# Kernel tuning notes

Measured on AMD Instinct MI355X. Metric: run time of the kernel, lower is better.

Reference implementation:

```python
import jax, jax.numpy as jnp
import numpy as np

N_NODES = 1024
HID = 128
NODE_D = 133
BOND_D = 14
E_HALF = 8192  # directed edges; doubled with reverses -> 16384


def setup_inputs() -> dict:
    key = jax.random.key(0)
    ks = jax.random.split(key, 24)

    x = jax.random.normal(ks[0], (N_NODES, NODE_D), jnp.float32)
    edge_attr = jax.random.normal(ks[1], (2 * E_HALF, BOND_D), jnp.float32)
    src = jax.random.randint(ks[2], (E_HALF,), 0, N_NODES)
    dst = jax.random.randint(ks[3], (E_HALF,), 0, N_NODES)
    # bidirectional edges so every edge has a reverse (as _rev_edge_index assumes)
    edge_index = jnp.stack([jnp.concatenate([src, dst]), jnp.concatenate([dst, src])]).astype(jnp.int32)
    rev_edge_index = jnp.concatenate([jnp.arange(E_HALF) + E_HALF, jnp.arange(E_HALF)]).astype(jnp.int32)

    dissociable_masks = (jax.random.uniform(ks[4], (N_NODES,)) < 0.1).astype(jnp.int32)
    pka_raw = jax.random.uniform(ks[5], (N_NODES,), minval=0.0, maxval=14.0)
    valid = jax.random.uniform(ks[6], (N_NODES,)) < (1.0 / 16.0)
    pka_values = jnp.where(valid, pka_raw, jnp.nan).astype(jnp.float32)

    def lin(k, fi, fo):
        return (jax.random.normal(k, (fi, fo)) / np.sqrt(fi)).astype(jnp.float32)

    z = lambda n: jnp.zeros((n,), jnp.float32)
    inp = dict(x=x, edge_attr=edge_attr, pka_values=pka_values,
               dissociable_masks=dissociable_masks, edge_index=edge_index,
               rev_edge_index=rev_edge_index,
               Wi=lin(ks[7], NODE_D + BOND_D, HID), bi=z(HID),
               Wh=lin(ks[8], HID, HID), bh=z(HID),
               Wo=lin(ks[9], NODE_D + HID, HID), bo=z(HID),
               Wnt=lin(ks[10], NODE_D, HID), bnt=z(HID),
               Wc1=lin(ks[11], HID, 256), bc1=z(256),
               Wc2=lin(ks[12], 256, 64), bc2=z(64),
               Wc3=lin(ks[13], 64, 2), bc3=z(2),
               Wr1=lin(ks[14], HID, 256), br1=z(256),
               Wr2=lin(ks[15], 256, 64), br2=z(64),
               Wr3=lin(ks[16], 64, 1), br3=z(1),
               Wg=lin(ks[17], HID, HID), bg=z(HID))
    return inp


def reference(x, edge_attr, pka_values, dissociable_masks, edge_index, rev_edge_index,
              Wi, bi, Wh, bh, Wo, bo, Wnt, bnt,
              Wc1, bc1, Wc2, bc2, Wc3, bc3,
              Wr1, br1, Wr2, br2, Wr3, br3, Wg, bg):
    n = x.shape[0]
    src, dst = edge_index[0], edge_index[1]

    # ---- BondMessagePassing (depth=3, dropout in eval mode) ----
    H0 = jnp.concatenate([x[src], edge_attr], axis=1) @ Wi + bi  # [E, HID]
    Ht = jax.nn.relu(H0)
    for _ in range(2):  # depth - 1 iterations
        agg = jax.ops.segment_sum(Ht, dst, num_segments=n)       # scatter-sum to dst
        M = agg[src] - Ht[rev_edge_index]                        # exclude reverse edge
        Ht = jax.nn.relu(H0 + M @ Wh + bh)
    agg = jax.ops.segment_sum(Ht, dst, num_segments=n)
    tx = x @ Wnt + bnt
    M = jnp.where(jnp.sum(agg, axis=1, keepdims=True) == 0, tx, agg)
    E = jax.nn.relu(jnp.concatenate([x, M], axis=1) @ Wo + bo)   # node embeddings [N, HID]

    valid = ~jnp.isnan(pka_values)
    pka_s = jnp.where(valid, pka_values, 0.0)

    def mlp(e, W1, b1, W2, b2, W3, b3):
        h = jax.nn.relu(e @ W1 + b1)
        h = jax.nn.relu(h @ W2 + b2)
        return h @ W3 + b3

    def step(carry, inp):
        Emb, cls_sum, reg_sum, correct = carry
        i, m_i, p_i, v_i = inp
        e = Emb[i]
        logits = mlp(e, Wc1, bc1, Wc2, bc2, Wc3, bc3)            # [2]
        label = jnp.argmax(logits).astype(jnp.int32)
        target = (m_i > 0).astype(jnp.int32)
        ce = -jax.nn.log_softmax(logits)[target]
        correct = correct + (label == target).astype(jnp.float32)
        reg_cond = (label == 1) | (m_i > 0)
        # sigmoid -> Hardtanh(0,14) (clip is identity on (0,1), kept for fidelity)
        p = jnp.clip(jax.nn.sigmoid(mlp(e, Wr1, br1, Wr2, br2, Wr3, br3))[0], 0.0, 14.0)
        fire = reg_cond & v_i
        reg_sum = reg_sum + jnp.where(fire, (p - p_i) ** 2, 0.0)
        Emb = jax.lax.cond(fire,
                           lambda A: A * (1.0 - jax.nn.sigmoid(A @ Wg + bg)),
                           lambda A: A, Emb)
        return (Emb, cls_sum + ce, reg_sum, correct), (label, jnp.where(reg_cond, p, 0.0))

    init = (E, jnp.float32(0.0), jnp.float32(0.0), jnp.float32(0.0))
    xs = (jnp.arange(n), dissociable_masks, pka_s, valid)
    (_, cls_sum, reg_sum, correct), (labels, preds) = jax.lax.scan(step, init, xs)
    acc = jax.lax.stop_gradient(correct / n)
    loss_vec = jnp.stack([cls_sum + reg_sum, cls_sum, reg_sum, acc])
    return labels, preds, loss_vec
```

## Files before the change

kernel.cpp:

```cpp
#include <hip/hip_runtime.h>

#define NN   1024
#define NE   16384
#define HID  128
#define ND   133
#define BD   14
#define KIN  147
#define NVMAX 128
#define EB   8
#define JF   4
#define JT   2
#define MAXPAIRS (NVMAX * (NVMAX + 1) / 2)
#define TB4 ((MAXPAIRS + JT - 1) / JT)

__device__ __forceinline__ float sigm(float x) { return 1.0f / (1.0f + expf(-x)); }


__global__ void __launch_bounds__(1024)
k_prep3(const int* __restrict__ dst, int* offs, int* elist,
        const float* __restrict__ pka, int* validIdx, int* NvP, int* vpos,
        const int* __restrict__ mask, int* pairCnt, int* pairList,
        int* lossTicket) {
    __shared__ int degS[NN];
    __shared__ int s2[NN];
    __shared__ int fillS[NN];
    __shared__ int elistS[NE];
    __shared__ int vIdxS[NVMAX];
    __shared__ int maskS[NVMAX];
    __shared__ int nvS, pcS;
    int t = threadIdx.x;
    degS[t] = 0;
    float v = pka[t];
    int f = (v == v) ? 1 : 0;
    s2[t] = f;
    __syncthreads();
    for (int e = t; e < NE; e += NN) atomicAdd(&degS[dst[e]], 1);
    __syncthreads();
    int d0 = degS[t];
    __syncthreads();
    for (int st = 1; st < NN; st <<= 1) {
        int a = (t >= st) ? degS[t - st] : 0;
        int b = (t >= st) ? s2[t - st] : 0;
        __syncthreads();
        degS[t] += a; s2[t] += b;
        __syncthreads();
    }
    int hi = degS[t];
    int lo = hi - d0;
    offs[t] = lo;
    fillS[t] = lo;
    if (t == NN - 1) offs[NN] = hi;
    int pos = s2[t] - f;
    int ok = (f && pos < NVMAX) ? 1 : 0;
    vpos[t] = ok ? pos : -1;
    if (ok) { validIdx[pos] = t; vIdxS[pos] = t; }
    if (t == NN - 1) { int nv = (s2[t] > NVMAX) ? NVMAX : s2[t]; *NvP = nv; nvS = nv; }
    if (t == 0) { pcS = 0; *lossTicket = 0; }
    __syncthreads();
    for (int e = t; e < NE; e += NN) { int p = atomicAdd(&fillS[dst[e]], 1); elistS[p] = e; }
    int Nv = nvS;
    if (t < NVMAX) maskS[t] = (t < Nv) ? mask[vIdxS[t]] : 1;
    __syncthreads();
    for (int a = lo + 1; a < hi; a++) {
        int vv = elistS[a]; int b = a - 1;
        while (b >= lo && elistS[b] > vv) { elistS[b + 1] = elistS[b]; b--; }
        elistS[b + 1] = vv;
    }
    for (int idx = t; idx < NVMAX * NVMAX; idx += NN) {
        int vv = idx >> 7, k = idx & (NVMAX - 1);
        if (vv < Nv && k <= vv && maskS[vv] == 0) {
            int p = atomicAdd(&pcS, 1);
            pairList[p] = idx;
        }
    }
    __syncthreads();
    if (t == 0) *pairCnt = pcS;
    for (int e = t; e < NE; e += NN) elist[e] = elistS[e];
}


__global__ void k_edge_init(const float* __restrict__ x, const float* __restrict__ ea,
                            const int* __restrict__ src,
                            const float* __restrict__ Wi, const float* __restrict__ bi,
                            float* __restrict__ H0, float* __restrict__ Ht) {
    __shared__ float in[EB][KIN + 1];
    int e0 = blockIdx.x * EB;
    int h = threadIdx.x;
    for (int j = 0; j < EB; j++) {
        int e = e0 + j; int s = src[e];
        for (int k = h; k < KIN; k += HID)
            in[j][k] = (k < ND) ? x[s * ND + k] : ea[e * BD + (k - ND)];
    }
    __syncthreads();
    float acc[EB];
#pragma unroll
    for (int j = 0; j < EB; j++) acc[j] = 0.f;
    for (int k = 0; k < KIN; k++) {
        float w = Wi[k * HID + h];
#pragma unroll
        for (int j = 0; j < EB; j++) acc[j] = fmaf(in[j][k], w, acc[j]);
    }
    float b = bi[h];
    for (int j = 0; j < EB; j++) {
        float v = acc[j] + b;
        H0[(e0 + j) * HID + h] = v;
        Ht[(e0 + j) * HID + h] = fmaxf(v, 0.f);
    }
}

__global__ void k_segsum(const float* __restrict__ Ht, const int* __restrict__ elist,
                         const int* __restrict__ offs, float* __restrict__ agg) {
    int n = blockIdx.x; int h = threadIdx.x;
    int lo = offs[n], hi = offs[n + 1];
    float a = 0.f;
    for (int j = lo; j < hi; j++) {
        int e = elist[j];
        a += Ht[e * HID + h];
    }
    agg[n * HID + h] = a;
}

__global__ void k_edge_update(const float* __restrict__ H0, const float* __restrict__ Htin,
                              const float* __restrict__ agg,
                              const int* __restrict__ src, const int* __restrict__ rev,
                              const float* __restrict__ Wh, const float* __restrict__ bh,
                              float* __restrict__ Htout) {
    __shared__ float M[EB][HID];
    int e0 = blockIdx.x * EB;
    int h = threadIdx.x;
    for (int j = 0; j < EB; j++) {
        int e = e0 + j; int s = src[e]; int r = rev[e];
        M[j][h] = agg[s * HID + h] - Htin[r * HID + h];
    }
    __syncthreads();
    float acc[EB];
#pragma unroll
    for (int j = 0; j < EB; j++) acc[j] = 0.f;
    for (int k = 0; k < HID; k++) {
        float w = Wh[k * HID + h];
#pragma unroll
        for (int j = 0; j < EB; j++) acc[j] = fmaf(M[j][k], w, acc[j]);
    }
    float b = bh[h];
    for (int j = 0; j < EB; j++) {
        int e = e0 + j;
        Htout[e * HID + h] = fmaxf(H0[e * HID + h] + acc[j] + b, 0.f);
    }
}

__global__ void k_node_embed2(const float* __restrict__ x, const float* __restrict__ Ht,
                              const int* __restrict__ elist, const int* __restrict__ offs,
                              const float* __restrict__ Wnt, const float* __restrict__ bnt,
                              const float* __restrict__ Wo, const float* __restrict__ bo,
                              float* __restrict__ Emb) {
    __shared__ float xs[ND + 1];
    __shared__ float Ms[HID];
    __shared__ float red[HID];
    int n = blockIdx.x; int h = threadIdx.x;
    for (int k = h; k < ND; k += HID) xs[k] = x[n * ND + k];
    int lo = offs[n], hi = offs[n + 1];
    float a = 0.f;
    for (int j = lo; j < hi; j++) a += Ht[elist[j] * HID + h];
    red[h] = a;
    __syncthreads();
    for (int st = 64; st > 0; st >>= 1) { if (h < st) red[h] += red[h + st]; __syncthreads(); }
    float s = red[0];
    __syncthreads();
    float Mh;
    if (s == 0.0f) {
        float t0 = 0.f, t1 = 0.f;
        int k = 0;
        for (; k + 1 < ND; k += 2) {
            t0 = fmaf(xs[k], Wnt[k * HID + h], t0);
            t1 = fmaf(xs[k + 1], Wnt[(k + 1) * HID + h], t1);
        }
        for (; k < ND; k++) t0 = fmaf(xs[k], Wnt[k * HID + h], t0);
        Mh = (t0 + t1) + bnt[h];
    } else {
        Mh = a;
    }
    Ms[h] = Mh;
    __syncthreads();
    float a0 = 0.f, a1 = 0.f;
    int k = 0;
    for (; k + 1 < ND; k += 2) {
        a0 = fmaf(xs[k], Wo[k * HID + h], a0);
        a1 = fmaf(xs[k + 1], Wo[(k + 1) * HID + h], a1);
    }
    for (; k < ND; k++) a0 = fmaf(xs[k], Wo[k * HID + h], a0);
    for (int q = 0; q < HID; q += 2) {
        a0 = fmaf(Ms[q], Wo[(ND + q) * HID + h], a0);
        a1 = fmaf(Ms[q + 1], Wo[(ND + q + 1) * HID + h], a1);
    }
    Emb[n * HID + h] = fmaxf((a0 + a1) + bo[h], 0.f);
}


__global__ void __launch_bounds__(512)
k_chains3(const float* __restrict__ Emb, const int* __restrict__ validIdx,
          const int* __restrict__ NvP,
          const float* __restrict__ Wg, const float* __restrict__ bg,
          float* __restrict__ specSt) {
    int v = blockIdx.x;
    int Nv = *NvP;
    if (v >= Nv) return;
    __shared__ float rS[HID];
    __shared__ float pS[512];
    int tid = threadIdx.x;
    int col = tid & (HID - 1);
    int slot = tid >> 7;
    float wreg[32];
#pragma unroll
    for (int q = 0; q < 32; q++)
        wreg[q] = Wg[(slot * 32 + q) * HID + col];
    float bgc = bg[col];
    int i = validIdx[v];
    if (tid < HID) rS[tid] = Emb[i * HID + tid];
    __syncthreads();
    if (slot == 0) specSt[(size_t)(v * NVMAX + 0) * HID + col] = rS[col];
    int kmax = (v < NVMAX - 1) ? v : (NVMAX - 1);
    for (int k = 1; k <= kmax; k++) {
        const float4* r4 = (const float4*)&rS[slot * 32];
        float px = 0.f, py = 0.f, pz = 0.f, pw = 0.f;
#pragma unroll
        for (int q8 = 0; q8 < 8; q8++) {
            float4 rr = r4[q8];
            px = fmaf(rr.x, wreg[4 * q8 + 0], px);
            py = fmaf(rr.y, wreg[4 * q8 + 1], py);
            pz = fmaf(rr.z, wreg[4 * q8 + 2], pz);
            pw = fmaf(rr.w, wreg[4 * q8 + 3], pw);
        }
        pS[tid] = (px + py) + (pz + pw);
        __syncthreads();
        if (slot == 0) {
            float s = ((pS[col] + pS[col + 128]) + (pS[col + 256] + pS[col + 384])) + bgc;
            float g = 1.0f - sigm(s);
            float nr = rS[col] * g;
            rS[col] = nr;
            specSt[(size_t)(v * NVMAX + k) * HID + col] = nr;
        }
        __syncthreads();
    }
}


__global__ void __launch_bounds__(256)
k_table4(const float* __restrict__ specSt, const int* __restrict__ pairList,
         const int* __restrict__ pairCnt,
         const float* __restrict__ Wc1, const float* __restrict__ bc1,
         const float* __restrict__ Wc2, const float* __restrict__ bc2,
         const float* __restrict__ Wc3, const float* __restrict__ bc3,
         int* __restrict__ labTab) {
    int cnt = *pairCnt;
    int base = blockIdx.x * JT;
    if (base >= cnt) return;
    int nj = cnt - base; if (nj > JT) nj = JT;
    __shared__ float rS[JT][HID];
    __shared__ float h1S[JT][256];
    __shared__ float h2S[JT][64];
    __shared__ int plS[JT];
    int tid = threadIdx.x;
    if (tid < JT) plS[tid] = (tid < nj) ? pairList[base + tid] : 0;
    __syncthreads();
    for (int idx = tid; idx < JT * HID; idx += 256) {
        int j = idx >> 7, k = idx & (HID - 1);
        rS[j][k] = (j < nj) ? specSt[(size_t)plS[j] * HID + k] : 0.f;
    }
    __syncthreads();
    {
        float a[JT];
#pragma unroll
        for (int j = 0; j < JT; j++) a[j] = 0.f;
        for (int k = 0; k < HID; k++) {
            float w = Wc1[k * 256 + tid];
#pragma unroll
            for (int j = 0; j < JT; j++) a[j] = fmaf(rS[j][k], w, a[j]);
        }
        float b1 = bc1[tid];
#pragma unroll
        for (int j = 0; j < JT; j++) h1S[j][tid] = fmaxf(a[j] + b1, 0.f);
    }
    __syncthreads();
    {
        int col = tid & 63, j = tid >> 6;
        if (j < nj) {
            float acc = 0.f;
            for (int k = 0; k < 256; k++)
                acc = fmaf(h1S[j][k], Wc2[k * 64 + col], acc);
            h2S[j][col] = fmaxf(acc + bc2[col], 0.f);
        }
    }
    __syncthreads();
    if (tid < nj) {
        float l0 = bc3[0], l1 = bc3[1];
        for (int k = 0; k < 64; k++) {
            float h = h2S[tid][k];
            l0 = fmaf(h, Wc3[2 * k + 0], l0);
            l1 = fmaf(h, Wc3[2 * k + 1], l1);
        }
        labTab[plS[tid]] = (l1 > l0) ? 1 : 0;
    }
}


__global__ void k_resolve2(const int* __restrict__ validIdx, const int* __restrict__ NvP,
                           const int* __restrict__ mask, const int* __restrict__ labTab,
                           int* fireFlag, int* kPref) {
    __shared__ int vIdxS[NVMAX];
    __shared__ int maskS[NVMAX];
    __shared__ int labS[NVMAX * NVMAX];
    __shared__ int fireS[NN];
    __shared__ int scanS[NN];
    int t = threadIdx.x;
    int Nv = *NvP;
    if (t < NVMAX) {
        int vi = (t < Nv) ? validIdx[t] : 0;
        vIdxS[t] = vi;
        maskS[t] = (t < Nv) ? mask[vi] : 0;
    }
    fireS[t] = 0;
    for (int idx = t; idx < Nv * NVMAX; idx += NN) labS[idx] = labTab[idx];
    __syncthreads();
    if (t == 0) {
        int k = 0;
        for (int v = 0; v < Nv; v++) {
            int fire = (maskS[v] > 0) ? 1 : labS[v * NVMAX + k];
            fireS[vIdxS[v]] = fire;
            k += fire;
        }
    }
    __syncthreads();
    int f0 = fireS[t];
    scanS[t] = f0;
    __syncthreads();
    for (int st = 1; st < NN; st <<= 1) {
        int u = (t >= st) ? scanS[t - st] : 0;
        __syncthreads();
        scanS[t] += u;
        __syncthreads();
    }
    kPref[t] = scanS[t] - f0;
    fireFlag[t] = f0;
}


__global__ void __launch_bounds__(256)
k_final4(const float* __restrict__ Emb, const int* __restrict__ kPref,
         const int* __restrict__ fireFlag, const int* __restrict__ mask,
         const float* __restrict__ pka, const int* __restrict__ vpos,
         const int* __restrict__ labTab,
         const float* __restrict__ Wg, const float* __restrict__ bg,
         const float* __restrict__ Wc1, const float* __restrict__ bc1,
         const float* __restrict__ Wc2, const float* __restrict__ bc2,
         const float* __restrict__ Wc3, const float* __restrict__ bc3,
         const float* __restrict__ Wr1, const float* __restrict__ br1,
         const float* __restrict__ Wr2, const float* __restrict__ br2,
         const float* __restrict__ Wr3, const float* __restrict__ br3,
         float* __restrict__ outLabels, float* __restrict__ outPreds,
         float* __restrict__ ceArr, float* __restrict__ regArr,
         float* __restrict__ corArr, float* __restrict__ outLoss,
         int* __restrict__ lossTicket) {
    __shared__ float WgS[HID * HID];
    __shared__ float rS[JF][HID];
    __shared__ float h1S[JF][256];
    __shared__ float h2S[JF][64];
    __shared__ float lgS[JF][2];
    __shared__ float prS[JF];
    __shared__ int kcS[JF];
    __shared__ int tkS;
    int tid = threadIdx.x;
    int i0 = blockIdx.x * JF;

    const float4* Wg4 = (const float4*)Wg;
    float4* Ws4 = (float4*)WgS;
    for (int idx = tid; idx < HID * HID / 4; idx += 256) Ws4[idx] = Wg4[idx];
    if (tid < HID) {
#pragma unroll
        for (int j = 0; j < JF; j++) rS[j][tid] = Emb[(i0 + j) * HID + tid];
    }
    if (tid < JF) kcS[tid] = kPref[i0 + tid];
    __syncthreads();
    int kc[JF]; int maxkc = 0;
#pragma unroll
    for (int j = 0; j < JF; j++) { kc[j] = kcS[j]; if (kc[j] > maxkc) maxkc = kc[j]; }

    int col = tid & (HID - 1);
    int slot = tid >> 7;
    int j0 = slot * 2, j1 = slot * 2 + 1;
    float bgc = bg[col];
    for (int t = 0; t < maxkc; t++) {
        float a00 = 0.f, a01 = 0.f, a02 = 0.f, a03 = 0.f;
        float a10 = 0.f, a11 = 0.f, a12 = 0.f, a13 = 0.f;
        for (int q = 0; q < HID; q += 4) {
            float w0 = WgS[(q + 0) * HID + col];
            float w1 = WgS[(q + 1) * HID + col];
            float w2 = WgS[(q + 2) * HID + col];
            float w3 = WgS[(q + 3) * HID + col];
            a00 = fmaf(rS[j0][q + 0], w0, a00);
            a01 = fmaf(rS[j0][q + 1], w1, a01);
            a02 = fmaf(rS[j0][q + 2], w2, a02);
            a03 = fmaf(rS[j0][q + 3], w3, a03);
            a10 = fmaf(rS[j1][q + 0], w0, a10);
            a11 = fmaf(rS[j1][q + 1], w1, a11);
            a12 = fmaf(rS[j1][q + 2], w2, a12);
            a13 = fmaf(rS[j1][q + 3], w3, a13);
        }
        float g0 = 1.0f - sigm(((a00 + a01) + (a02 + a03)) + bgc);
        float g1 = 1.0f - sigm(((a10 + a11) + (a12 + a13)) + bgc);
        __syncthreads();
        if (t < kc[j0]) rS[j0][col] *= g0;
        if (t < kc[j1]) rS[j1][col] *= g1;
        __syncthreads();
    }

    {
        float a[JF];
#pragma unroll
        for (int j = 0; j < JF; j++) a[j] = 0.f;
        for (int k = 0; k < HID; k++) {
            float w = Wc1[k * 256 + tid];
#pragma unroll
            for (int j = 0; j < JF; j++) a[j] = fmaf(rS[j][k], w, a[j]);
        }
        float b = bc1[tid];
#pragma unroll
        for (int j = 0; j < JF; j++) h1S[j][tid] = fmaxf(a[j] + b, 0.f);
    }
    __syncthreads();
    {
        int c2 = tid & 63, j = tid >> 6;
        float acc = 0.f;
        for (int k = 0; k < 256; k++) acc = fmaf(h1S[j][k], Wc2[k * 64 + c2], acc);
        h2S[j][c2] = fmaxf(acc + bc2[c2], 0.f);
    }
    __syncthreads();
    if (tid < 2 * JF) {
        int j = tid >> 1, c = tid & 1;
        float l = bc3[c];
        for (int k = 0; k < 64; k++) l = fmaf(h2S[j][k], Wc3[2 * k + c], l);
        lgS[j][c] = l;
    }
    __syncthreads();

    {
        float a[JF];
#pragma unroll
        for (int j = 0; j < JF; j++) a[j] = 0.f;
        for (int k = 0; k < HID; k++) {
            float w = Wr1[k * 256 + tid];
#pragma unroll
            for (int j = 0; j < JF; j++) a[j] = fmaf(rS[j][k], w, a[j]);
        }
        float b = br1[tid];
#pragma unroll
        for (int j = 0; j < JF; j++) h1S[j][tid] = fmaxf(a[j] + b, 0.f);
    }
    __syncthreads();
    {
        int c2 = tid & 63, j = tid >> 6;
        float acc = 0.f;
        for (int k = 0; k < 256; k++) acc = fmaf(h1S[j][k], Wr2[k * 64 + c2], acc);
        h2S[j][c2] = fmaxf(acc + br2[c2], 0.f);
    }
    __syncthreads();
    if (tid < JF) {
        float pr = br3[0];
        for (int k = 0; k < 64; k++) pr = fmaf(h2S[tid][k], Wr3[k], pr);
        prS[tid] = pr;
    }
    __syncthreads();

    if (tid < JF) {
        int j = tid, i = i0 + j;
        float l0 = lgS[j][0], l1 = lgS[j][1];
        int compLab = (l1 > l0) ? 1 : 0;
        int vp = vpos[i];
        int label = (vp >= 0 && mask[i] == 0) ? labTab[vp * NVMAX + kc[j]] : compLab;
        int target = (mask[i] > 0) ? 1 : 0;
        float mx = fmaxf(l0, l1);
        float lse = mx + logf(expf(l0 - mx) + expf(l1 - mx));
        float ce = lse - ((target == 1) ? l1 : l0);
        int reg_cond = (label == 1) || (mask[i] > 0);
        float p = sigm(prS[j]);
        p = fminf(fmaxf(p, 0.f), 14.f);
        outLabels[i] = (float)label;
        outPreds[i] = reg_cond ? p : 0.f;
        ceArr[i] = ce;
        corArr[i] = (label == target) ? 1.f : 0.f;
        if (fireFlag[i]) {
            float d = p - pka[i];
            regArr[i] = d * d;
        } else {
            regArr[i] = 0.f;
        }
    }

    __threadfence();
    __syncthreads();
    if (tid == 0) tkS = atomicAdd(lossTicket, 1);
    __syncthreads();
    if (tkS == (NN / JF) - 1) {
        __threadfence();
        __shared__ float s[256];
        float a = ((ceArr[tid] + ceArr[tid + 256]) + (ceArr[tid + 512] + ceArr[tid + 768]));
        s[tid] = a; __syncthreads();
        for (int st = 128; st > 0; st >>= 1) { if (tid < st) s[tid] += s[tid + st]; __syncthreads(); }
        float cls = s[0]; __syncthreads();
        a = ((regArr[tid] + regArr[tid + 256]) + (regArr[tid + 512] + regArr[tid + 768]));
        s[tid] = a; __syncthreads();
        for (int st = 128; st > 0; st >>= 1) { if (tid < st) s[tid] += s[tid + st]; __syncthreads(); }
        float reg = s[0]; __syncthreads();
        a = ((corArr[tid] + corArr[tid + 256]) + (corArr[tid + 512] + corArr[tid + 768]));
        s[tid] = a; __syncthreads();
        for (int st = 128; st > 0; st >>= 1) { if (tid < st) s[tid] += s[tid + st]; __syncthreads(); }
        float cor = s[0];
        if (tid == 0) {
            outLoss[0] = cls + reg;
            outLoss[1] = cls;
            outLoss[2] = reg;
            outLoss[3] = cor / (float)NN;
        }
    }
}


extern "C" void kernel_launch(void* const* d_in, const int* in_sizes, int n_in,
                              void* d_out, int out_size, void* d_ws, size_t ws_size,
                              hipStream_t stream) {
    const float* x    = (const float*)d_in[0];
    const float* ea   = (const float*)d_in[1];
    const float* pka  = (const float*)d_in[2];
    const int*   mask = (const int*)d_in[3];
    const int*   eidx = (const int*)d_in[4];
    const int*   rev  = (const int*)d_in[5];
    const float* Wi  = (const float*)d_in[6];  const float* bi  = (const float*)d_in[7];
    const float* Wh  = (const float*)d_in[8];  const float* bh  = (const float*)d_in[9];
    const float* Wo  = (const float*)d_in[10]; const float* bo  = (const float*)d_in[11];
    const float* Wnt = (const float*)d_in[12]; const float* bnt = (const float*)d_in[13];
    const float* Wc1 = (const float*)d_in[14]; const float* bc1 = (const float*)d_in[15];
    const float* Wc2 = (const float*)d_in[16]; const float* bc2 = (const float*)d_in[17];
    const float* Wc3 = (const float*)d_in[18]; const float* bc3 = (const float*)d_in[19];
    const float* Wr1 = (const float*)d_in[20]; const float* br1 = (const float*)d_in[21];
    const float* Wr2 = (const float*)d_in[22]; const float* br2 = (const float*)d_in[23];
    const float* Wr3 = (const float*)d_in[24]; const float* br3 = (const float*)d_in[25];
    const float* Wg  = (const float*)d_in[26]; const float* bg  = (const float*)d_in[27];

    const int* src = eidx;
    const int* dst = eidx + NE;

    char* w = (char*)d_ws;
    auto alloc = [&](size_t bytes) -> void* {
        void* p = (void*)w;
        w += ((bytes + 255) / 256) * 256;
        return p;
    };
    float* H0   = (float*)alloc((size_t)NE * HID * 4);
    float* HtA  = (float*)alloc((size_t)NE * HID * 4);
    float* HtB  = (float*)alloc((size_t)NE * HID * 4);
    float* agg  = (float*)alloc((size_t)NN * HID * 4);
    float* Emb  = (float*)alloc((size_t)NN * HID * 4);
    int* offs    = (int*)alloc((NN + 1) * 4);
    int* elist   = (int*)alloc(NE * 4);
    int* validIdx= (int*)alloc(NVMAX * 4);
    int* NvP     = (int*)alloc(16);
    int* vpos    = (int*)alloc(NN * 4);
    int* fireFlag= (int*)alloc(NN * 4);
    int* kPref   = (int*)alloc(NN * 4);
    float* specSt= (float*)alloc((size_t)NVMAX * NVMAX * HID * 4);
    int* labTab  = (int*)alloc(NVMAX * NVMAX * 4);
    int* pairCnt = (int*)alloc(16);
    int* pairList= (int*)alloc(MAXPAIRS * 4);
    int* lossTicket = (int*)alloc(16);
    float* ceArr = (float*)alloc(NN * 4);
    float* regArr= (float*)alloc(NN * 4);
    float* corArr= (float*)alloc(NN * 4);

    float* outF = (float*)d_out;

    k_prep3<<<1, NN, 0, stream>>>(dst, offs, elist, pka, validIdx, NvP, vpos,
                                  mask, pairCnt, pairList, lossTicket);

    k_edge_init<<<NE / EB, HID, 0, stream>>>(x, ea, src, Wi, bi, H0, HtA);
    k_segsum<<<NN, HID, 0, stream>>>(HtA, elist, offs, agg);
    k_edge_update<<<NE / EB, HID, 0, stream>>>(H0, HtA, agg, src, rev, Wh, bh, HtB);
    k_segsum<<<NN, HID, 0, stream>>>(HtB, elist, offs, agg);
    k_edge_update<<<NE / EB, HID, 0, stream>>>(H0, HtB, agg, src, rev, Wh, bh, HtA);
    k_node_embed2<<<NN, HID, 0, stream>>>(x, HtA, elist, offs, Wnt, bnt, Wo, bo, Emb);

    k_chains3<<<NVMAX, 512, 0, stream>>>(Emb, validIdx, NvP, Wg, bg, specSt);
    k_table4<<<TB4, 256, 0, stream>>>(specSt, pairList, pairCnt,
                                      Wc1, bc1, Wc2, bc2, Wc3, bc3, labTab);
    k_resolve2<<<1, NN, 0, stream>>>(validIdx, NvP, mask, labTab, fireFlag, kPref);

    k_final4<<<NN / JF, 256, 0, stream>>>(Emb, kPref, fireFlag, mask, pka, vpos, labTab,
                                          Wg, bg, Wc1, bc1, Wc2, bc2, Wc3, bc3,
                                          Wr1, br1, Wr2, br2, Wr3, br3,
                                          outF, outF + NN, ceArr, regArr, corArr,
                                          outF + 2 * NN, lossTicket);
}
```

Baseline: 223.3 us.

## Hold Wg gate weights in registers and split final kernel into smaller blocks

```diff
diff --git a/kernel.cpp b/kernel.cpp
--- a/kernel.cpp
+++ b/kernel.cpp
@@ -8,10 +8,11 @@
 #define KIN  147
 #define NVMAX 128
 #define EB   8
-#define JF   4
+#define JF   2
 #define JT   2
 #define MAXPAIRS (NVMAX * (NVMAX + 1) / 2)
 #define TB4 ((MAXPAIRS + JT - 1) / JT)
+#define FB  (NN / JF)
 
 __device__ __forceinline__ float sigm(float x) { return 1.0f / (1.0f + expf(-x)); }
 
@@ -344,8 +345,8 @@
 }
 
 
-__global__ void __launch_bounds__(256)
-k_final4(const float* __restrict__ Emb, const int* __restrict__ kPref,
+__global__ void __launch_bounds__(512)
+k_final5(const float* __restrict__ Emb, const int* __restrict__ kPref,
          const int* __restrict__ fireFlag, const int* __restrict__ mask,
          const float* __restrict__ pka, const int* __restrict__ vpos,
          const int* __restrict__ labTab,
@@ -360,8 +361,8 @@
          float* __restrict__ ceArr, float* __restrict__ regArr,
          float* __restrict__ corArr, float* __restrict__ outLoss,
          int* __restrict__ lossTicket) {
-    __shared__ float WgS[HID * HID];
     __shared__ float rS[JF][HID];
+    __shared__ float pS[512];
     __shared__ float h1S[JF][256];
     __shared__ float h2S[JF][64];
     __shared__ float lgS[JF][2];
@@ -371,67 +372,61 @@
     int tid = threadIdx.x;
     int i0 = blockIdx.x * JF;
 
-    const float4* Wg4 = (const float4*)Wg;
-    float4* Ws4 = (float4*)WgS;
-    for (int idx = tid; idx < HID * HID / 4; idx += 256) Ws4[idx] = Wg4[idx];
-    if (tid < HID) {
-#pragma unroll
-        for (int j = 0; j < JF; j++) rS[j][tid] = Emb[(i0 + j) * HID + tid];
+    int gj   = tid >> 8;
+    int half = (tid >> 7) & 1;
+    int gcol = tid & (HID - 1);
+    float wreg[64];
+#pragma unroll
+    for (int q = 0; q < 64; q++)
+        wreg[q] = Wg[(half * 64 + q) * HID + gcol];
+
+    if (tid < JF * HID) {
+        int j = tid >> 7, c = tid & (HID - 1);
+        rS[j][c] = Emb[(i0 + j) * HID + c];
     }
     if (tid < JF) kcS[tid] = kPref[i0 + tid];
     __syncthreads();
-    int kc[JF]; int maxkc = 0;
-#pragma unroll
-    for (int j = 0; j < JF; j++) { kc[j] = kcS[j]; if (kc[j] > maxkc) maxkc = kc[j]; }
-
-    int col = tid & (HID - 1);
-    int slot = tid >> 7;
-    int j0 = slot * 2, j1 = slot * 2 + 1;
-    float bgc = bg[col];
+    int kc0 = kcS[0], kc1 = kcS[1];
+    int maxkc = (kc0 > kc1) ? kc0 : kc1;
+
+    float bgc = bg[gcol];
+
     for (int t = 0; t < maxkc; t++) {
-        float a00 = 0.f, a01 = 0.f, a02 = 0.f, a03 = 0.f;
-        float a10 = 0.f, a11 = 0.f, a12 = 0.f, a13 = 0.f;
-        for (int q = 0; q < HID; q += 4) {
-            float w0 = WgS[(q + 0) * HID + col];
-            float w1 = WgS[(q + 1) * HID + col];
-            float w2 = WgS[(q + 2) * HID + col];
-            float w3 = WgS[(q + 3) * HID + col];
-            a00 = fmaf(rS[j0][q + 0], w0, a00);
-            a01 = fmaf(rS[j0][q + 1], w1, a01);
-            a02 = fmaf(rS[j0][q + 2], w2, a02);
-            a03 = fmaf(rS[j0][q + 3], w3, a03);
-            a10 = fmaf(rS[j1][q + 0], w0, a10);
-            a11 = fmaf(rS[j1][q + 1], w1, a11);
-            a12 = fmaf(rS[j1][q + 2], w2, a12);
-            a13 = fmaf(rS[j1][q + 3], w3, a13);
-        }
-        float g0 = 1.0f - sigm(((a00 + a01) + (a02 + a03)) + bgc);
-        float g1 = 1.0f - sigm(((a10 + a11) + (a12 + a13)) + bgc);
-        __syncthreads();
-        if (t < kc[j0]) rS[j0][col] *= g0;
-        if (t < kc[j1]) rS[j1][col] *= g1;
+        const float4* r4 = (const float4*)&rS[gj][half * 64];
+        float px = 0.f, py = 0.f, pz = 0.f, pw = 0.f;
+#pragma unroll
+        for (int q4 = 0; q4 < 16; q4++) {
+            float4 rr = r4[q4];
+            px = fmaf(rr.x, wreg[4 * q4 + 0], px);
+            py = fmaf(rr.y, wreg[4 * q4 + 1], py);
+            pz = fmaf(rr.z, wreg[4 * q4 + 2], pz);
+            pw = fmaf(rr.w, wreg[4 * q4 + 3], pw);
+        }
+        pS[tid] = (px + py) + (pz + pw);
+        __syncthreads();
+        if (tid < 256) {
+            int j = tid >> 7, col = tid & (HID - 1);
+            float s = (pS[j * 256 + col] + pS[j * 256 + 128 + col]) + bgc;
+            float g = 1.0f - sigm(s);
+            int kcj = (j == 0) ? kc0 : kc1;
+            if (t < kcj) rS[j][col] *= g;
+        }
         __syncthreads();
     }
 
     {
-        float a[JF];
-#pragma unroll
-        for (int j = 0; j < JF; j++) a[j] = 0.f;
-        for (int k = 0; k < HID; k++) {
-            float w = Wc1[k * 256 + tid];
-#pragma unroll
-            for (int j = 0; j < JF; j++) a[j] = fmaf(rS[j][k], w, a[j]);
-        }
-        float b = bc1[tid];
-#pragma unroll
-        for (int j = 0; j < JF; j++) h1S[j][tid] = fmaxf(a[j] + b, 0.f);
-    }
-    __syncthreads();
-    {
-        int c2 = tid & 63, j = tid >> 6;
+        int j = tid >> 8, c = tid & 255;
+        float a = 0.f;
+        for (int k = 0; k < HID; k++)
+            a = fmaf(rS[j][k], Wc1[k * 256 + c], a);
+        h1S[j][c] = fmaxf(a + bc1[c], 0.f);
+    }
+    __syncthreads();
+    if (tid < JF * 64) {
+        int j = tid >> 6, c = tid & 63;
         float acc = 0.f;
-        for (int k = 0; k < 256; k++) acc = fmaf(h1S[j][k], Wc2[k * 64 + c2], acc);
-        h2S[j][c2] = fmaxf(acc + bc2[c2], 0.f);
+        for (int k = 0; k < 256; k++) acc = fmaf(h1S[j][k], Wc2[k * 64 + c], acc);
+        h2S[j][c] = fmaxf(acc + bc2[c], 0.f);
     }
     __syncthreads();
     if (tid < 2 * JF) {
@@ -443,24 +438,18 @@
     __syncthreads();
 
     {
-        float a[JF];
-#pragma unroll
-        for (int j = 0; j < JF; j++) a[j] = 0.f;
-        for (int k = 0; k < HID; k++) {
-            float w = Wr1[k * 256 + tid];
-#pragma unroll
-            for (int j = 0; j < JF; j++) a[j] = fmaf(rS[j][k], w, a[j]);
-        }
-        float b = br1[tid];
-#pragma unroll
-        for (int j = 0; j < JF; j++) h1S[j][tid] = fmaxf(a[j] + b, 0.f);
-    }
-    __syncthreads();
-    {
-        int c2 = tid & 63, j = tid >> 6;
+        int j = tid >> 8, c = tid & 255;
+        float a = 0.f;
+        for (int k = 0; k < HID; k++)
+            a = fmaf(rS[j][k], Wr1[k * 256 + c], a);
+        h1S[j][c] = fmaxf(a + br1[c], 0.f);
+    }
+    __syncthreads();
+    if (tid < JF * 64) {
+        int j = tid >> 6, c = tid & 63;
         float acc = 0.f;
-        for (int k = 0; k < 256; k++) acc = fmaf(h1S[j][k], Wr2[k * 64 + c2], acc);
-        h2S[j][c2] = fmaxf(acc + br2[c2], 0.f);
+        for (int k = 0; k < 256; k++) acc = fmaf(h1S[j][k], Wr2[k * 64 + c], acc);
+        h2S[j][c] = fmaxf(acc + br2[c], 0.f);
     }
     __syncthreads();
     if (tid < JF) {
@@ -472,10 +461,11 @@
 
     if (tid < JF) {
         int j = tid, i = i0 + j;
+        int kcj = (j == 0) ? kc0 : kc1;
         float l0 = lgS[j][0], l1 = lgS[j][1];
         int compLab = (l1 > l0) ? 1 : 0;
         int vp = vpos[i];
-        int label = (vp >= 0 && mask[i] == 0) ? labTab[vp * NVMAX + kc[j]] : compLab;
+        int label = (vp >= 0 && mask[i] == 0) ? labTab[vp * NVMAX + kcj] : compLab;
         int target = (mask[i] > 0) ? 1 : 0;
         float mx = fmaxf(l0, l1);
         float lse = mx + logf(expf(l0 - mx) + expf(l1 - mx));
@@ -499,20 +489,20 @@
     __syncthreads();
     if (tid == 0) tkS = atomicAdd(lossTicket, 1);
     __syncthreads();
-    if (tkS == (NN / JF) - 1) {
+    if (tkS == FB - 1) {
         __threadfence();
-        __shared__ float s[256];
-        float a = ((ceArr[tid] + ceArr[tid + 256]) + (ceArr[tid + 512] + ceArr[tid + 768]));
+        __shared__ float s[512];
+        float a = ceArr[tid] + ceArr[tid + 512];
         s[tid] = a; __syncthreads();
-        for (int st = 128; st > 0; st >>= 1) { if (tid < st) s[tid] += s[tid + st]; __syncthreads(); }
+        for (int st = 256; st > 0; st >>= 1) { if (tid < st) s[tid] += s[tid + st]; __syncthreads(); }
         float cls = s[0]; __syncthreads();
-        a = ((regArr[tid] + regArr[tid + 256]) + (regArr[tid + 512] + regArr[tid + 768]));
+        a = regArr[tid] + regArr[tid + 512];
         s[tid] = a; __syncthreads();
-        for (int st = 128; st > 0; st >>= 1) { if (tid < st) s[tid] += s[tid + st]; __syncthreads(); }
+        for (int st = 256; st > 0; st >>= 1) { if (tid < st) s[tid] += s[tid + st]; __syncthreads(); }
         float reg = s[0]; __syncthreads();
-        a = ((corArr[tid] + corArr[tid + 256]) + (corArr[tid + 512] + corArr[tid + 768]));
+        a = corArr[tid] + corArr[tid + 512];
         s[tid] = a; __syncthreads();
-        for (int st = 128; st > 0; st >>= 1) { if (tid < st) s[tid] += s[tid + st]; __syncthreads(); }
+        for (int st = 256; st > 0; st >>= 1) { if (tid < st) s[tid] += s[tid + st]; __syncthreads(); }
         float cor = s[0];
         if (tid == 0) {
             outLoss[0] = cls + reg;
@@ -592,9 +582,9 @@
                                       Wc1, bc1, Wc2, bc2, Wc3, bc3, labTab);
     k_resolve2<<<1, NN, 0, stream>>>(validIdx, NvP, mask, labTab, fireFlag, kPref);
 
-    k_final4<<<NN / JF, 256, 0, stream>>>(Emb, kPref, fireFlag, mask, pka, vpos, labTab,
-                                          Wg, bg, Wc1, bc1, Wc2, bc2, Wc3, bc3,
-                                          Wr1, br1, Wr2, br2, Wr3, br3,
-                                          outF, outF + NN, ceArr, regArr, corArr,
-                                          outF + 2 * NN, lossTicket);
-}
+    k_final5<<<FB, 512, 0, stream>>>(Emb, kPref, fireFlag, mask, pka, vpos, labTab,
+                                     Wg, bg, Wc1, bc1, Wc2, bc2, Wc3, bc3,
+                                     Wr1, br1, Wr2, br2, Wr3, br3,
+                                     outF, outF + NN, ceArr, regArr, corArr,
+                                     outF + 2 * NN, lossTicket);
+}
```

New measurement: 262.9 us. 1.18x slower.
